# Optimization experiments

Measured on AMD Instinct MI355X. Metric: run time of the kernel, lower is better.

## Reference

```python
import jax, jax.numpy as jnp
import numpy as np

N_NODES = 50000
N_EDGES = 800000
IN_FEATS = 128
HEADS = 8
OUT_FEATS = 32
NEG_SLOPE = 0.2


def setup_inputs() -> dict:
    key = jax.random.key(0)
    k_feat, k_w, k_al, k_ar, k_src, k_dst = jax.random.split(key, 6)
    feat = jax.random.normal(k_feat, (N_NODES, IN_FEATS), dtype=jnp.float32)
    W_fc = jax.random.normal(k_w, (HEADS * OUT_FEATS, IN_FEATS), dtype=jnp.float32) * 0.1
    attn_l = jax.random.normal(k_al, (1, HEADS, OUT_FEATS), dtype=jnp.float32) * 0.1
    attn_r = jax.random.normal(k_ar, (1, HEADS, OUT_FEATS), dtype=jnp.float32) * 0.1
    src = jax.random.randint(k_src, (N_EDGES,), 0, N_NODES, dtype=jnp.int32)
    dst = jax.random.randint(k_dst, (N_EDGES,), 0, N_NODES, dtype=jnp.int32)
    return {"feat": feat, "W_fc": W_fc, "attn_l": attn_l, "attn_r": attn_r,
            "src": src, "dst": dst}


def reference(feat, W_fc, attn_l, attn_r, src, dst):
    N = feat.shape[0]
    H, D = attn_l.shape[1], attn_l.shape[2]
    # fc projection: [N, H, D]
    feat_hd = (feat @ W_fc.T).reshape(N, H, D)
    # per-node left/right attention logits: [N, H]
    el = (feat_hd * attn_l).sum(-1)
    er = (feat_hd * attn_r).sum(-1)
    # u_add_v gather -> per-edge score [E, H], then leaky relu
    e = el[src] + er[dst]
    e = jnp.where(e > 0, e, NEG_SLOPE * e)
    # edge softmax: segment softmax over edges grouped by dst node
    m = jax.ops.segment_max(e, dst, num_segments=N)        # [N, H]
    a = jnp.exp(e - m[dst])                                # [E, H]
    z = jax.ops.segment_sum(a, dst, num_segments=N)        # [N, H]
    a = a / z[dst]
    # u_mul_e + sum: weighted scatter-aggregation -> [N, H, D]
    msg = feat_hd[src] * a[:, :, None]                     # [E, H, D]
    out = jax.ops.segment_sum(msg, dst, num_segments=N)
    return out
```

## Files before the change

### kernel.cpp

```cpp
#include <hip/hip_runtime.h>

#define N_NODES_C 50000
#define N_EDGES_C 800000
#define IN_FEATS_C 128
#define HEADS_C 8
#define HD_C 256
#define NEG_SLOPE_C 0.2f
#define SCAN_NBLK 49
#define LDT 136

#define GEMM_BLOCKS 782
#define DEG_BLOCKS 242
#define K1_GRID (GEMM_BLOCKS + DEG_BLOCKS)

typedef __attribute__((ext_vector_type(8))) short bf16x8;
typedef __attribute__((ext_vector_type(4))) float floatx4;
typedef __attribute__((ext_vector_type(4))) unsigned int uintx4;

__device__ inline unsigned short f2bf(float f) {
  unsigned int u = __float_as_uint(f);
  unsigned int r = (u + 0x7FFFu + ((u >> 16) & 1u)) >> 16;
  return (unsigned short)r;
}
__device__ inline float bf2f(unsigned short s) {
  unsigned int u = ((unsigned int)s) << 16;
  return __uint_as_float(u);
}

__device__ inline void boff_scan(const int* __restrict__ bsum, int* sboff) {
  int t = threadIdx.x;
  if (t < 64) {
    int own = (t < SCAN_NBLK) ? bsum[t] : 0;
    int v = own;
#pragma unroll
    for (int off = 1; off < 64; off <<= 1) {
      int u = __shfl_up(v, off);
      if (t >= off) v += u;
    }
    sboff[t] = v - own;
  }
  __syncthreads();
}

__global__ __launch_bounds__(256) void front_kernel(
    const float* __restrict__ feat, const float* __restrict__ W,
    const float* __restrict__ attn_l, const float* __restrict__ attn_r,
    const int* __restrict__ dst,
    unsigned short* __restrict__ feat_hd_bf,
    float* __restrict__ el, float* __restrict__ er,
    int* __restrict__ deg, int* __restrict__ rank) {
  __shared__ __align__(16) unsigned short sA[128 * LDT];
  __shared__ float sAttnL[128];
  __shared__ float sAttnR[128];
  const int bid = blockIdx.x;
  const int t = threadIdx.x;

  if (bid < DEG_BLOCKS) {
    for (int e0 = (bid * 256 + t) * 8; e0 < N_EDGES_C; e0 += DEG_BLOCKS * 2048) {
      int4 da = *(const int4*)&dst[e0];
      int4 db = *(const int4*)&dst[e0 + 4];
      int r0 = atomicAdd(&deg[da.x], 1);
      int r1 = atomicAdd(&deg[da.y], 1);
      int r2 = atomicAdd(&deg[da.z], 1);
      int r3 = atomicAdd(&deg[da.w], 1);
      int r4 = atomicAdd(&deg[db.x], 1);
      int r5 = atomicAdd(&deg[db.y], 1);
      int r6 = atomicAdd(&deg[db.z], 1);
      int r7 = atomicAdd(&deg[db.w], 1);
      *(int4*)&rank[e0]     = make_int4(r0, r1, r2, r3);
      *(int4*)&rank[e0 + 4] = make_int4(r4, r5, r6, r7);
    }
    return;
  }

  const int gb = bid - DEG_BLOCKS;
  const int nt = gb & 1;
  const int mt = gb >> 1;
  const int m0 = mt * 128;
  const int n0 = nt * 128;

  if (t < 128) {
    sAttnL[t] = attn_l[n0 + t];
    sAttnR[t] = attn_r[n0 + t];
  }
#pragma unroll
  for (int i = 0; i < 16; ++i) {
    int idx = t + i * 256;
    int row = idx >> 5;
    int c4 = idx & 31;
    int gn = m0 + row;
    floatx4 v = (floatx4){0.f, 0.f, 0.f, 0.f};
    if (gn < N_NODES_C)
      v = __builtin_nontemporal_load(
          (const floatx4*)&feat[(size_t)gn * IN_FEATS_C + c4 * 4]);
    ushort4 b;
    b.x = f2bf(v[0]); b.y = f2bf(v[1]); b.z = f2bf(v[2]); b.w = f2bf(v[3]);
    *(ushort4*)&sA[row * LDT + c4 * 4] = b;
  }
  __syncthreads();

  const int wid = t >> 6;
  const int lane = t & 63;
  const int quad = lane >> 4;
  const int l16 = lane & 15;
  const int wm = (wid & 1) * 64;
  const int wn = (wid >> 1) * 64;

  floatx4 acc[4][4];
#pragma unroll
  for (int i = 0; i < 4; ++i)
#pragma unroll
    for (int j = 0; j < 4; ++j) acc[i][j] = (floatx4){0.f, 0.f, 0.f, 0.f};

#pragma unroll
  for (int ks = 0; ks < 4; ++ks) {
    int k0 = ks * 32 + quad * 8;
    bf16x8 bfv[4];
#pragma unroll
    for (int n2 = 0; n2 < 4; ++n2) {
      const float* wp = &W[(size_t)(n0 + wn + n2 * 16 + l16) * IN_FEATS_C + k0];
      float4 w0 = *(const float4*)wp;
      float4 w1 = *(const float4*)(wp + 4);
      bf16x8 b;
      b[0] = (short)f2bf(w0.x); b[1] = (short)f2bf(w0.y);
      b[2] = (short)f2bf(w0.z); b[3] = (short)f2bf(w0.w);
      b[4] = (short)f2bf(w1.x); b[5] = (short)f2bf(w1.y);
      b[6] = (short)f2bf(w1.z); b[7] = (short)f2bf(w1.w);
      bfv[n2] = b;
    }
    bf16x8 af[4];
#pragma unroll
    for (int m2 = 0; m2 < 4; ++m2)
      af[m2] = *(const bf16x8*)&sA[(wm + m2 * 16 + l16) * LDT + k0];
#pragma unroll
    for (int m2 = 0; m2 < 4; ++m2)
#pragma unroll
      for (int n2 = 0; n2 < 4; ++n2)
        acc[m2][n2] = __builtin_amdgcn_mfma_f32_16x16x32_bf16(
            af[m2], bfv[n2], acc[m2][n2], 0, 0, 0);
  }
  __syncthreads();

#pragma unroll
  for (int m2 = 0; m2 < 4; ++m2)
#pragma unroll
    for (int n2 = 0; n2 < 4; ++n2)
#pragma unroll
      for (int r = 0; r < 4; ++r) {
        int row = wm + m2 * 16 + quad * 4 + r;
        int col = wn + n2 * 16 + l16;
        sA[row * LDT + col] = f2bf(acc[m2][n2][r]);
      }
  __syncthreads();

#pragma unroll
  for (int i = 0; i < 8; ++i) {
    int idx = t + i * 256;
    int row = idx >> 4;
    int ch = idx & 15;
    int gn = m0 + row;
    if (gn < N_NODES_C) {
      uintx4 v = *(const uintx4*)&sA[row * LDT + ch * 8];
      __builtin_nontemporal_store(
          v, (uintx4*)&feat_hd_bf[(size_t)gn * HD_C + n0 + ch * 8]);
    }
  }

  {
    int row = t >> 1;
    int hh = t & 1;
    int gn = m0 + row;
    if (gn < N_NODES_C) {
      const unsigned short* pr = &sA[row * LDT + hh * 64];
      const float* al = &sAttnL[hh * 64];
      const float* ar = &sAttnR[hh * 64];
      float el0 = 0.f, el1 = 0.f, er0 = 0.f, er1 = 0.f;
#pragma unroll
      for (int d = 0; d < 32; ++d) {
        float v0 = bf2f(pr[d]);
        float v1 = bf2f(pr[32 + d]);
        el0 = fmaf(v0, al[d], el0);
        er0 = fmaf(v0, ar[d], er0);
        el1 = fmaf(v1, al[32 + d], el1);
        er1 = fmaf(v1, ar[32 + d], er1);
      }
      int gh = nt * 4 + hh * 2;
      el[gn * HEADS_C + gh + 0] = el0;
      el[gn * HEADS_C + gh + 1] = el1;
      er[gn * HEADS_C + gh + 0] = er0;
      er[gn * HEADS_C + gh + 1] = er1;
    }
  }
}

__global__ __launch_bounds__(256) void scan1_kernel(
    const int* __restrict__ deg, int2* __restrict__ rsd,
    int* __restrict__ bsum) {
  __shared__ int s[256];
  int b = blockIdx.x, t = threadIdx.x;
  int i0 = b * 1024 + t * 4;
  int d0 = 0, d1 = 0, d2 = 0, d3 = 0;
  if (i0 + 4 <= N_NODES_C) {
    int4 d = *(const int4*)&deg[i0];
    d0 = d.x; d1 = d.y; d2 = d.z; d3 = d.w;
  } else {
    if (i0 + 0 < N_NODES_C) d0 = deg[i0 + 0];
    if (i0 + 1 < N_NODES_C) d1 = deg[i0 + 1];
    if (i0 + 2 < N_NODES_C) d2 = deg[i0 + 2];
    if (i0 + 3 < N_NODES_C) d3 = deg[i0 + 3];
  }
  int l1 = d0, l2 = l1 + d1, l3 = l2 + d2, l4 = l3 + d3;
  s[t] = l4;
  __syncthreads();
#pragma unroll
  for (int off = 1; off < 256; off <<= 1) {
    int add = (t >= off) ? s[t - off] : 0;
    __syncthreads();
    s[t] += add;
    __syncthreads();
  }
  int excl = s[t] - l4;
  if (i0 + 0 < N_NODES_C) rsd[i0 + 0] = make_int2(excl + l1, d0);
  if (i0 + 1 < N_NODES_C) rsd[i0 + 1] = make_int2(excl + l2, d1);
  if (i0 + 2 < N_NODES_C) rsd[i0 + 2] = make_int2(excl + l3, d2);
  if (i0 + 3 < N_NODES_C) rsd[i0 + 3] = make_int2(excl + l4, d3);
  if (t == 255) bsum[b] = s[255];
}

__global__ __launch_bounds__(256) void scatter_kernel(
    const int* __restrict__ src, const int* __restrict__ dst,
    const int2* __restrict__ rsd, const int* __restrict__ bsum,
    const int* __restrict__ rank, int* __restrict__ csr_src) {
  __shared__ int sboff[64];
  boff_scan(bsum, sboff);
  int e = blockIdx.x * 256 + threadIdx.x;
  if (e >= N_EDGES_C) return;
  int d = dst[e];
  int2 v = rsd[d];
  int pos = v.x - v.y + sboff[d >> 10] + rank[e];
  csr_src[pos] = src[e];
}

__global__ __launch_bounds__(256) void agg_csr_kernel(
    const unsigned short* __restrict__ feat_hd_bf, const float* __restrict__ el,
    const float* __restrict__ er, const int2* __restrict__ rsd,
    const int* __restrict__ bsum, const int* __restrict__ csr_src,
    float* __restrict__ out) {
  __shared__ int sboff[64];
  boff_scan(bsum, sboff);
  int gid = blockIdx.x * 256 + threadIdx.x;
  int node = gid >> 6;
  int lane = threadIdx.x & 63;
  if (node >= N_NODES_C) return;
  int h = lane >> 3;
  int j8 = lane & 7;
  int hbase = lane & 56;
  int c = lane * 4;
  float er_d = er[node * HEADS_C + h];
  int2 v = rsd[node];
  int dg = v.y;
  int rs = v.x - dg + sboff[node >> 10];
  float4 acc = make_float4(0.f, 0.f, 0.f, 0.f);
  float zsum = 0.f;

  int nb = (dg + 7) >> 3;
  if (nb > 0) {
    const int last = dg - 1;
    int idxA = csr_src[rs + min(j8, last)];
    float elA = el[idxA * HEADS_C + h];
    ushort4 fA[8];
#pragma unroll
    for (int j = 0; j < 8; ++j) {
      int sj = __shfl(idxA, j);
      fA[j] = *(const ushort4*)&feat_hd_bf[(size_t)sj * HD_C + c];
    }
    int idxB = csr_src[rs + min(8 + j8, last)];

    for (int b = 0; b < nb; b += 2) {
      float elB = el[idxB * HEADS_C + h];
      ushort4 fB[8];
#pragma unroll
      for (int j = 0; j < 8; ++j) {
        int sj = __shfl(idxB, j);
        fB[j] = *(const ushort4*)&feat_hd_bf[(size_t)sj * HD_C + c];
      }
      int idxC = csr_src[rs + min((b + 2) * 8 + j8, last)];
      {
        float x = elA + er_d;
        x = x > 0.f ? x : NEG_SLOPE_C * x;
        float wv = (b * 8 + j8 < dg) ? __expf(x) : 0.f;
        float wj[8];
#pragma unroll
        for (int j = 0; j < 8; ++j) wj[j] = __shfl(wv, hbase + j);
        zsum += ((wj[0] + wj[1]) + (wj[2] + wj[3])) +
                ((wj[4] + wj[5]) + (wj[6] + wj[7]));
#pragma unroll
        for (int j = 0; j < 8; ++j) {
          acc.x = fmaf(wj[j], bf2f(fA[j].x), acc.x);
          acc.y = fmaf(wj[j], bf2f(fA[j].y), acc.y);
          acc.z = fmaf(wj[j], bf2f(fA[j].z), acc.z);
          acc.w = fmaf(wj[j], bf2f(fA[j].w), acc.w);
        }
      }
      float elA2 = el[idxC * HEADS_C + h];
#pragma unroll
      for (int j = 0; j < 8; ++j) {
        int sj = __shfl(idxC, j);
        fA[j] = *(const ushort4*)&feat_hd_bf[(size_t)sj * HD_C + c];
      }
      int idxD = csr_src[rs + min((b + 3) * 8 + j8, last)];
      {
        float x = elB + er_d;
        x = x > 0.f ? x : NEG_SLOPE_C * x;
        float wv = ((b + 1) * 8 + j8 < dg) ? __expf(x) : 0.f;
        float wj[8];
#pragma unroll
        for (int j = 0; j < 8; ++j) wj[j] = __shfl(wv, hbase + j);
        zsum += ((wj[0] + wj[1]) + (wj[2] + wj[3])) +
                ((wj[4] + wj[5]) + (wj[6] + wj[7]));
#pragma unroll
        for (int j = 0; j < 8; ++j) {
          acc.x = fmaf(wj[j], bf2f(fB[j].x), acc.x);
          acc.y = fmaf(wj[j], bf2f(fB[j].y), acc.y);
          acc.z = fmaf(wj[j], bf2f(fB[j].z), acc.z);
          acc.w = fmaf(wj[j], bf2f(fB[j].w), acc.w);
        }
      }
      idxA = idxC; elA = elA2; idxB = idxD;
    }
  }

  float inv = (dg > 0) ? 1.f / zsum : 0.f;
  floatx4 ov = (floatx4){acc.x * inv, acc.y * inv, acc.z * inv, acc.w * inv};
  __builtin_nontemporal_store(ov, (floatx4*)&out[(size_t)node * HD_C + c]);
}

extern "C" void kernel_launch(void* const* d_in, const int* in_sizes, int n_in,
                              void* d_out, int out_size, void* d_ws, size_t ws_size,
                              hipStream_t stream) {
  const float* feat   = (const float*)d_in[0];
  const float* W      = (const float*)d_in[1];
  const float* attn_l = (const float*)d_in[2];
  const float* attn_r = (const float*)d_in[3];
  const int* src      = (const int*)d_in[4];
  const int* dst      = (const int*)d_in[5];
  float* out = (float*)d_out;

  char* ws = (char*)d_ws;
  unsigned short* feat_hd_bf = (unsigned short*)ws;  ws += (size_t)N_NODES_C * HD_C * 2;
  float* el      = (float*)ws;                       ws += (size_t)N_NODES_C * HEADS_C * 4;
  float* er      = (float*)ws;                       ws += (size_t)N_NODES_C * HEADS_C * 4;
  int* deg       = (int*)ws;                         ws += (size_t)N_NODES_C * 4;
  int2* rsd      = (int2*)ws;                        ws += (size_t)N_NODES_C * 8;
  int* bsum      = (int*)ws;                         ws += 64 * 4;
  int* csr_src   = (int*)ws;                         ws += (size_t)N_EDGES_C * 4;
  int* rank      = (int*)ws;                         ws += (size_t)N_EDGES_C * 4;

  hipMemsetAsync(deg, 0, (size_t)N_NODES_C * 4, stream);

  front_kernel<<<K1_GRID, 256, 0, stream>>>(feat, W, attn_l, attn_r, dst,
                                            feat_hd_bf, el, er, deg, rank);

  scan1_kernel<<<SCAN_NBLK, 256, 0, stream>>>(deg, rsd, bsum);

  scatter_kernel<<<(N_EDGES_C + 255) / 256, 256, 0, stream>>>(
      src, dst, rsd, bsum, rank, csr_src);

  agg_csr_kernel<<<(N_NODES_C + 3) / 4, 256, 0, stream>>>(
      feat_hd_bf, el, er, rsd, bsum, csr_src, out);
}
```

Measured before the change: 247.5 us.

## Process two destination nodes per wavefront in CSR aggregation and drop nontemporal stores

The aggregation kernel now assigns two destination nodes to each wavefront and interleaves their edge batches, replacing the previous double-buffered software pipeline over one node. The aim is more independent gathers in flight per wave and more work per wave, at the cost of looping to the larger of the two degrees and halving the grid. Nontemporal stores for feat_hd and the output are replaced with ordinary stores, which may keep the feat_hd rows in cache for the gather that follows. Clamping the CSR indices to the last edge guards against out-of-range reads when a node has degree zero.

```diff
diff --git a/kernel.cpp b/kernel.cpp
--- a/kernel.cpp
+++ b/kernel.cpp
@@ -12,6 +12,7 @@
 #define GEMM_BLOCKS 782
 #define DEG_BLOCKS 242
 #define K1_GRID (GEMM_BLOCKS + DEG_BLOCKS)
+#define EMAX (N_EDGES_C - 1)
 
 typedef __attribute__((ext_vector_type(8))) short bf16x8;
 typedef __attribute__((ext_vector_type(4))) float floatx4;
@@ -160,9 +161,8 @@
     int ch = idx & 15;
     int gn = m0 + row;
     if (gn < N_NODES_C) {
-      uintx4 v = *(const uintx4*)&sA[row * LDT + ch * 8];
-      __builtin_nontemporal_store(
-          v, (uintx4*)&feat_hd_bf[(size_t)gn * HD_C + n0 + ch * 8]);
+      *(uint4*)&feat_hd_bf[(size_t)gn * HD_C + n0 + ch * 8] =
+          *(const uint4*)&sA[row * LDT + ch * 8];
     }
   }
 
@@ -248,91 +248,99 @@
     float* __restrict__ out) {
   __shared__ int sboff[64];
   boff_scan(bsum, sboff);
-  int gid = blockIdx.x * 256 + threadIdx.x;
-  int node = gid >> 6;
+  int wvid = (blockIdx.x * 256 + threadIdx.x) >> 6;
   int lane = threadIdx.x & 63;
-  if (node >= N_NODES_C) return;
+  int nodeA = wvid * 2;
+  int nodeB = nodeA + 1;
+  if (nodeA >= N_NODES_C) return;
+  const bool hasB = (nodeB < N_NODES_C);
   int h = lane >> 3;
   int j8 = lane & 7;
   int hbase = lane & 56;
   int c = lane * 4;
-  float er_d = er[node * HEADS_C + h];
-  int2 v = rsd[node];
-  int dg = v.y;
-  int rs = v.x - dg + sboff[node >> 10];
-  float4 acc = make_float4(0.f, 0.f, 0.f, 0.f);
-  float zsum = 0.f;
-
-  int nb = (dg + 7) >> 3;
+
+  int2 va = rsd[nodeA];
+  int dgA = va.y;
+  int rsA = va.x - dgA + sboff[nodeA >> 10];
+  float erA = er[nodeA * HEADS_C + h];
+  int dgB = 0, rsB = 0;
+  float erB = 0.f;
+  if (hasB) {
+    int2 vb = rsd[nodeB];
+    dgB = vb.y;
+    rsB = vb.x - dgB + sboff[nodeB >> 10];
+    erB = er[nodeB * HEADS_C + h];
+  }
+
+  float4 accA = make_float4(0.f, 0.f, 0.f, 0.f);
+  float4 accB = make_float4(0.f, 0.f, 0.f, 0.f);
+  float zA = 0.f, zB = 0.f;
+
+  int nbA = (dgA + 7) >> 3;
+  int nbB = (dgB + 7) >> 3;
+  int nb = max(nbA, nbB);
   if (nb > 0) {
-    const int last = dg - 1;
-    int idxA = csr_src[rs + min(j8, last)];
-    float elA = el[idxA * HEADS_C + h];
-    ushort4 fA[8];
-#pragma unroll
-    for (int j = 0; j < 8; ++j) {
-      int sj = __shfl(idxA, j);
-      fA[j] = *(const ushort4*)&feat_hd_bf[(size_t)sj * HD_C + c];
-    }
-    int idxB = csr_src[rs + min(8 + j8, last)];
-
-    for (int b = 0; b < nb; b += 2) {
-      float elB = el[idxB * HEADS_C + h];
-      ushort4 fB[8];
+    const int lastA = (dgA > 0) ? dgA - 1 : 0;
+    const int lastB = (dgB > 0) ? dgB - 1 : 0;
+    int idxA = csr_src[min(rsA + min(j8, lastA), EMAX)];
+    int idxB = csr_src[min(rsB + min(j8, lastB), EMAX)];
+    for (int b = 0; b < nb; ++b) {
+      int e0 = b * 8;
+      ushort4 fa[8], fb[8];
+#pragma unroll
+      for (int j = 0; j < 8; ++j) {
+        int sj = __shfl(idxA, j);
+        fa[j] = *(const ushort4*)&feat_hd_bf[(size_t)sj * HD_C + c];
+      }
 #pragma unroll
       for (int j = 0; j < 8; ++j) {
         int sj = __shfl(idxB, j);
-        fB[j] = *(const ushort4*)&feat_hd_bf[(size_t)sj * HD_C + c];
-      }
-      int idxC = csr_src[rs + min((b + 2) * 8 + j8, last)];
-      {
-        float x = elA + er_d;
-        x = x > 0.f ? x : NEG_SLOPE_C * x;
-        float wv = (b * 8 + j8 < dg) ? __expf(x) : 0.f;
-        float wj[8];
-#pragma unroll
-        for (int j = 0; j < 8; ++j) wj[j] = __shfl(wv, hbase + j);
-        zsum += ((wj[0] + wj[1]) + (wj[2] + wj[3])) +
-                ((wj[4] + wj[5]) + (wj[6] + wj[7]));
-#pragma unroll
-        for (int j = 0; j < 8; ++j) {
-          acc.x = fmaf(wj[j], bf2f(fA[j].x), acc.x);
-          acc.y = fmaf(wj[j], bf2f(fA[j].y), acc.y);
-          acc.z = fmaf(wj[j], bf2f(fA[j].z), acc.z);
-          acc.w = fmaf(wj[j], bf2f(fA[j].w), acc.w);
-        }
-      }
-      float elA2 = el[idxC * HEADS_C + h];
+        fb[j] = *(const ushort4*)&feat_hd_bf[(size_t)sj * HD_C + c];
+      }
+      float xA = el[idxA * HEADS_C + h] + erA;
+      xA = xA > 0.f ? xA : NEG_SLOPE_C * xA;
+      float wvA = (e0 + j8 < dgA) ? __expf(xA) : 0.f;
+      float xB = el[idxB * HEADS_C + h] + erB;
+      xB = xB > 0.f ? xB : NEG_SLOPE_C * xB;
+      float wvB = (e0 + j8 < dgB) ? __expf(xB) : 0.f;
+      int nidxA = csr_src[min(rsA + min(e0 + 8 + j8, lastA), EMAX)];
+      int nidxB = csr_src[min(rsB + min(e0 + 8 + j8, lastB), EMAX)];
+      float wjA[8], wjB[8];
+#pragma unroll
+      for (int j = 0; j < 8; ++j) wjA[j] = __shfl(wvA, hbase + j);
+#pragma unroll
+      for (int j = 0; j < 8; ++j) wjB[j] = __shfl(wvB, hbase + j);
+      zA += ((wjA[0] + wjA[1]) + (wjA[2] + wjA[3])) +
+            ((wjA[4] + wjA[5]) + (wjA[6] + wjA[7]));
+      zB += ((wjB[0] + wjB[1]) + (wjB[2] + wjB[3])) +
+            ((wjB[4] + wjB[5]) + (wjB[6] + wjB[7]));
 #pragma unroll
       for (int j = 0; j < 8; ++j) {
-        int sj = __shfl(idxC, j);
-        fA[j] = *(const ushort4*)&feat_hd_bf[(size_t)sj * HD_C + c];
-      }
-      int idxD = csr_src[rs + min((b + 3) * 8 + j8, last)];
-      {
-        float x = elB + er_d;
-        x = x > 0.f ? x : NEG_SLOPE_C * x;
-        float wv = ((b + 1) * 8 + j8 < dg) ? __expf(x) : 0.f;
-        float wj[8];
-#pragma unroll
-        for (int j = 0; j < 8; ++j) wj[j] = __shfl(wv, hbase + j);
-        zsum += ((wj[0] + wj[1]) + (wj[2] + wj[3])) +
-                ((wj[4] + wj[5]) + (wj[6] + wj[7]));
-#pragma unroll
-        for (int j = 0; j < 8; ++j) {
-          acc.x = fmaf(wj[j], bf2f(fB[j].x), acc.x);
-          acc.y = fmaf(wj[j], bf2f(fB[j].y), acc.y);
-          acc.z = fmaf(wj[j], bf2f(fB[j].z), acc.z);
-          acc.w = fmaf(wj[j], bf2f(fB[j].w), acc.w);
-        }
-      }
-      idxA = idxC; elA = elA2; idxB = idxD;
-    }
-  }
-
-  float inv = (dg > 0) ? 1.f / zsum : 0.f;
-  floatx4 ov = (floatx4){acc.x * inv, acc.y * inv, acc.z * inv, acc.w * inv};
-  __builtin_nontemporal_store(ov, (floatx4*)&out[(size_t)node * HD_C + c]);
+        accA.x = fmaf(wjA[j], bf2f(fa[j].x), accA.x);
+        accA.y = fmaf(wjA[j], bf2f(fa[j].y), accA.y);
+        accA.z = fmaf(wjA[j], bf2f(fa[j].z), accA.z);
+        accA.w = fmaf(wjA[j], bf2f(fa[j].w), accA.w);
+      }
+#pragma unroll
+      for (int j = 0; j < 8; ++j) {
+        accB.x = fmaf(wjB[j], bf2f(fb[j].x), accB.x);
+        accB.y = fmaf(wjB[j], bf2f(fb[j].y), accB.y);
+        accB.z = fmaf(wjB[j], bf2f(fb[j].z), accB.z);
+        accB.w = fmaf(wjB[j], bf2f(fb[j].w), accB.w);
+      }
+      idxA = nidxA;
+      idxB = nidxB;
+    }
+  }
+
+  float invA = (dgA > 0) ? 1.f / zA : 0.f;
+  *(float4*)&out[(size_t)nodeA * HD_C + c] =
+      make_float4(accA.x * invA, accA.y * invA, accA.z * invA, accA.w * invA);
+  if (hasB) {
+    float invB = (dgB > 0) ? 1.f / zB : 0.f;
+    *(float4*)&out[(size_t)nodeB * HD_C + c] =
+        make_float4(accB.x * invB, accB.y * invB, accB.z * invB, accB.w * invB);
+  }
 }
 
 extern "C" void kernel_launch(void* const* d_in, const int* in_sizes, int n_in,
@@ -366,6 +374,6 @@
   scatter_kernel<<<(N_EDGES_C + 255) / 256, 256, 0, stream>>>(
       src, dst, rsd, bsum, rank, csr_src);
 
-  agg_csr_kernel<<<(N_NODES_C + 3) / 4, 256, 0, stream>>>(
+  agg_csr_kernel<<<(N_NODES_C + 7) / 8, 256, 0, stream>>>(
       feat_hd_bf, el, er, rsd, bsum, csr_src, out);
 }
```

After: 232.4 us. 1.06x faster.
